# Kernel optimization log

Measured on AMD Instinct MI355X. Metric: run time of the kernel, lower is better.

The kernel has to match this reference:

```python
import jax, jax.numpy as jnp
import numpy as np

N_NODES = 50000
N_EDGES = 1600000
D = 128  # in_dim = hidden = out_dim = 128


def _gat_layer(x, W, b, aW, ab, src, dst, n_nodes):
    # fc: z = x @ W^T + b   (torch Linear convention, W:[out,in])
    z = x @ W.T + b                      # [N, d]
    d = z.shape[1]
    # attn_fc(concat(z_src, z_dst)) decomposed into per-node halves
    a_src = z @ aW[0, :d]                # [N]
    a_dst = z @ aW[0, d:]                # [N]
    e = jax.nn.leaky_relu(a_src[src] + a_dst[dst] + ab[0])  # [E], slope 0.01 (torch default)
    # segment softmax over incoming edges of each dst node
    m = jax.ops.segment_max(e, dst, num_segments=n_nodes)   # [N]
    ex = jnp.exp(e - m[dst])             # [E]
    s = jax.ops.segment_sum(ex, dst, num_segments=n_nodes)  # [N]
    alpha = ex / s[dst]                  # [E]
    # weighted scatter-sum of source features
    h = jax.ops.segment_sum(alpha[:, None] * z[src], dst, num_segments=n_nodes)  # [N, d]
    return h


def setup_inputs() -> dict:
    key = jax.random.key(0)
    ks = jax.random.split(key, 16)
    x = jax.random.normal(ks[0], (N_NODES, D), dtype=jnp.float32)
    src = jax.random.randint(ks[1], (N_EDGES,), 0, N_NODES, dtype=jnp.int32)
    dst = jax.random.randint(ks[2], (N_EDGES,), 0, N_NODES, dtype=jnp.int32)
    inp = {"x": x, "src": src, "dst": dst, "t": 0}
    # 3 GAT layers (128->128, 128->128, 128->128); xavier-ish scale
    for i in range(3):
        base = 3 + 4 * i
        inp[f"W{i}"] = jax.random.normal(ks[base], (D, D), dtype=jnp.float32) * (1.0 / np.sqrt(D))
        inp[f"b{i}"] = jnp.zeros((D,), dtype=jnp.float32)
        inp[f"aW{i}"] = jax.random.normal(ks[base + 1], (1, 2 * D), dtype=jnp.float32) * (1.0 / np.sqrt(2 * D))
        inp[f"ab{i}"] = jnp.zeros((1,), dtype=jnp.float32)
    return inp


def reference(x, src, dst, t, W0, b0, aW0, ab0, W1, b1, aW1, ab1, W2, b2, aW2, ab2):
    n = x.shape[0]
    h = _gat_layer(x, W0, b0, aW0, ab0, src, dst, n)
    h = jax.nn.relu(h)
    h = _gat_layer(h, W1, b1, aW1, ab1, src, dst, n)
    h = jax.nn.relu(h)
    h = _gat_layer(h, W2, b2, aW2, ab2, src, dst, n)
    return h
```

## Files before the change

kernel.cpp:

```cpp
#include <hip/hip_runtime.h>
#include <hip/hip_fp16.h>
#include <math.h>

#define DD 128
#define NBKT 391
#define P1CHUNK 4096
#define P2CAP 8192

typedef _Float16 half8 __attribute__((ext_vector_type(8)));
typedef float floatx4 __attribute__((ext_vector_type(4)));


__global__ __launch_bounds__(256) void fill_zero_i(int* p, int n) {
    int i = blockIdx.x * 256 + threadIdx.x;
    if (i < n) p[i] = 0;
}


__global__ __launch_bounds__(256) void cvt_k(const float* __restrict__ X, __half* __restrict__ Xh, int n8) {
    int i = blockIdx.x * 256 + threadIdx.x;
    if (i >= n8) return;
    const float4* p = reinterpret_cast<const float4*>(X + (size_t)i * 8);
    float4 v0 = p[0], v1 = p[1];
    __half hv[8];
    hv[0] = __float2half(v0.x); hv[1] = __float2half(v0.y);
    hv[2] = __float2half(v0.z); hv[3] = __float2half(v0.w);
    hv[4] = __float2half(v1.x); hv[5] = __float2half(v1.y);
    hv[6] = __float2half(v1.z); hv[7] = __float2half(v1.w);
    *reinterpret_cast<int4*>(Xh + (size_t)i * 8) = *reinterpret_cast<const int4*>(hv);
}

__global__ __launch_bounds__(256) void cvtw3_k(const float* __restrict__ W0, const float* __restrict__ W1,
                                               const float* __restrict__ W2, __half* __restrict__ Wh3) {
    int i = blockIdx.x * 256 + threadIdx.x;
    if (i >= 2048) return;
    const float* Ws[3] = {W0, W1, W2};
#pragma unroll
    for (int m = 0; m < 3; ++m) {
        const float4* p = reinterpret_cast<const float4*>(Ws[m] + (size_t)i * 8);
        float4 v0 = p[0], v1 = p[1];
        __half hv[8];
        hv[0] = __float2half(v0.x); hv[1] = __float2half(v0.y);
        hv[2] = __float2half(v0.z); hv[3] = __float2half(v0.w);
        hv[4] = __float2half(v1.x); hv[5] = __float2half(v1.y);
        hv[6] = __float2half(v1.z); hv[7] = __float2half(v1.w);
        *reinterpret_cast<int4*>(Wh3 + (size_t)m * 16384 + (size_t)i * 8) = *reinterpret_cast<const int4*>(hv);
    }
}


__global__ __launch_bounds__(512) void p1hist_k(const int* __restrict__ dst, int* __restrict__ gcount, int E) {
    __shared__ int lh[NBKT];
    const int tid = threadIdx.x;
    for (int i = tid; i < NBKT; i += 512) lh[i] = 0;
    __syncthreads();
    const int blk0 = blockIdx.x * P1CHUNK;
    const int blkE = min(blk0 + P1CHUNK, E);
    int i0 = blk0 + tid * 8;
    if (i0 + 8 <= blkE) {
        int4 d0 = *reinterpret_cast<const int4*>(dst + i0);
        int4 d1 = *reinterpret_cast<const int4*>(dst + i0 + 4);
        atomicAdd(&lh[d0.x >> 7], 1); atomicAdd(&lh[d0.y >> 7], 1);
        atomicAdd(&lh[d0.z >> 7], 1); atomicAdd(&lh[d0.w >> 7], 1);
        atomicAdd(&lh[d1.x >> 7], 1); atomicAdd(&lh[d1.y >> 7], 1);
        atomicAdd(&lh[d1.z >> 7], 1); atomicAdd(&lh[d1.w >> 7], 1);
    } else {
        for (int j = 0; j < 8; ++j) {
            int i = i0 + j;
            if (i < blkE) atomicAdd(&lh[dst[i] >> 7], 1);
        }
    }
    __syncthreads();
    for (int i = tid; i < NBKT; i += 512)
        if (lh[i]) atomicAdd(&gcount[i], lh[i]);
}


__global__ __launch_bounds__(512) void p1scan_k(const int* __restrict__ gcount, int* __restrict__ bbase,
                                                int* __restrict__ bcur, int E) {
    __shared__ int tmp[512];
    int t = threadIdx.x;
    int v = (t < NBKT) ? gcount[t] : 0;
    tmp[t] = v;
    __syncthreads();
#pragma unroll
    for (int o = 1; o < 512; o <<= 1) {
        int add = (t >= o) ? tmp[t - o] : 0;
        __syncthreads();
        tmp[t] += add;
        __syncthreads();
    }
    if (t <= NBKT) {
        int ex = (t < NBKT) ? (tmp[t] - v) : E;
        bbase[t] = ex;
        if (t < NBKT) bcur[t] = ex;
    }
}


__global__ __launch_bounds__(512) void p1scatter_k(const int* __restrict__ src, const int* __restrict__ dst,
                                                   int* __restrict__ bcur, int2* __restrict__ bufA, int E) {
    __shared__ int lcnt[NBKT];
    __shared__ int lstart[512];
    __shared__ int blkb[NBKT];
    __shared__ int2 stage[P1CHUNK];
    const int tid = threadIdx.x;
    for (int i = tid; i < NBKT; i += 512) lcnt[i] = 0;
    __syncthreads();
    const int blk0 = blockIdx.x * P1CHUNK;
    const int blkE = min(blk0 + P1CHUNK, E);
    const int i0 = blk0 + tid * 8;

    int sv[8], dv[8], bn[8], rk[8], cntT = 0;
    if (i0 + 8 <= blkE) {
        int4 s0 = *reinterpret_cast<const int4*>(src + i0);
        int4 s1 = *reinterpret_cast<const int4*>(src + i0 + 4);
        int4 d0 = *reinterpret_cast<const int4*>(dst + i0);
        int4 d1 = *reinterpret_cast<const int4*>(dst + i0 + 4);
        sv[0] = s0.x; sv[1] = s0.y; sv[2] = s0.z; sv[3] = s0.w;
        sv[4] = s1.x; sv[5] = s1.y; sv[6] = s1.z; sv[7] = s1.w;
        dv[0] = d0.x; dv[1] = d0.y; dv[2] = d0.z; dv[3] = d0.w;
        dv[4] = d1.x; dv[5] = d1.y; dv[6] = d1.z; dv[7] = d1.w;
        cntT = 8;
    } else {
#pragma unroll
        for (int j = 0; j < 8; ++j) {
            int i = i0 + j;
            if (i < blkE) { sv[j] = src[i]; dv[j] = dst[i]; cntT = j + 1; }
        }
    }
#pragma unroll
    for (int j = 0; j < 8; ++j) {
        if (j < cntT) {
            bn[j] = dv[j] >> 7;
            rk[j] = atomicAdd(&lcnt[bn[j]], 1);
        }
    }
    __syncthreads();
    int v = (tid < NBKT) ? lcnt[tid] : 0;
    lstart[tid] = v;
    __syncthreads();
#pragma unroll
    for (int o = 1; o < 512; o <<= 1) {
        int add = (tid >= o) ? lstart[tid - o] : 0;
        __syncthreads();
        lstart[tid] += add;
        __syncthreads();
    }
    lstart[tid] -= v;
    __syncthreads();
    for (int i = tid; i < NBKT; i += 512)
        blkb[i] = lcnt[i] ? atomicAdd(&bcur[i], lcnt[i]) : 0;
#pragma unroll
    for (int j = 0; j < 8; ++j) {
        if (j < cntT) {
            int pos = lstart[bn[j]] + rk[j];
            stage[pos] = make_int2(sv[j], dv[j]);
        }
    }
    __syncthreads();
    const int cnt = blkE - blk0;
    for (int j = tid; j < cnt; j += 512) {
        int2 e = stage[j];
        int b = e.y >> 7;
        bufA[blkb[b] + (j - lstart[b])] = e;
    }
}


__global__ __launch_bounds__(512) void p2sort_k(const int2* __restrict__ bufA, const int* __restrict__ bbase,
                                                int* __restrict__ srcs, int* __restrict__ off, int N, int E) {
    __shared__ int h2[128];
    __shared__ int cur2[128];
    __shared__ int ssrc[P2CAP];
    __shared__ int sdst[P2CAP];
    const int tid = threadIdx.x;
    const int b = blockIdx.x;
    const int base = bbase[b];
    const int cnt = bbase[b + 1] - base;
    for (int i = tid; i < 128; i += 512) h2[i] = 0;
    __syncthreads();
    for (int j = tid; j < cnt; j += 512)
        atomicAdd(&h2[bufA[base + j].y & 127], 1);
    __syncthreads();
    if (tid == 0) {
        int s = 0;
        for (int i = 0; i < 128; ++i) { cur2[i] = s; s += h2[i]; }
    }
    __syncthreads();
    for (int j = tid; j < cnt; j += 512) {
        int2 e = bufA[base + j];
        int p = atomicAdd(&cur2[e.y & 127], 1);
        ssrc[p] = e.x;
        sdst[p] = e.y;
    }
    __syncthreads();
    const int n0 = b * 128;
    const int n1 = min(n0 + 128, N);
    for (int j = tid; j < cnt; j += 512) {
        srcs[base + j] = ssrc[j];
        int d = sdst[j];
        int p = (j == 0) ? (n0 - 1) : sdst[j - 1];
        for (int n = p + 1; n <= d; ++n) off[n] = base + j;
        if (j == cnt - 1)
            for (int n = d + 1; n < n1; ++n) off[n] = base + cnt;
    }
    if (cnt == 0)
        for (int n = n0 + tid; n < n1; n += 512) off[n] = base;
    if (b == NBKT - 1 && tid == 0) off[N] = E;
}


__global__ __launch_bounds__(256) void gemm_k(const __half* __restrict__ Xh, const __half* __restrict__ Wh,
                                              const float* __restrict__ B, const float* __restrict__ aW,
                                              __half* __restrict__ Zh, float* __restrict__ a_src,
                                              float* __restrict__ a_dst, int N) {
    const int tid = threadIdx.x;
    const int wid = tid >> 6;
    const int lane = tid & 63;
    const int cl = lane & 15;
    const int kg = lane >> 4;
    const int row0 = blockIdx.x * 64 + wid * 16;
    int rowA = row0 + cl;
    if (rowA >= N) rowA = N - 1;

    floatx4 acc[8];
#pragma unroll
    for (int t = 0; t < 8; ++t) acc[t] = {0.f, 0.f, 0.f, 0.f};

    const _Float16* Xp = reinterpret_cast<const _Float16*>(Xh);
    const _Float16* Wp = reinterpret_cast<const _Float16*>(Wh);
#pragma unroll
    for (int kk = 0; kk < 4; ++kk) {
        const int kb = kk * 32 + kg * 8;
        half8 av = *reinterpret_cast<const half8*>(Xp + (size_t)rowA * 128 + kb);
#pragma unroll
        for (int t = 0; t < 8; ++t) {
            half8 bv = *reinterpret_cast<const half8*>(Wp + (size_t)(t * 16 + cl) * 128 + kb);
            acc[t] = __builtin_amdgcn_mfma_f32_16x16x32_f16(av, bv, acc[t], 0, 0, 0);
        }
    }
    float pa[4] = {0.f, 0.f, 0.f, 0.f}, pb[4] = {0.f, 0.f, 0.f, 0.f};
#pragma unroll
    for (int t = 0; t < 8; ++t) {
        const int c = t * 16 + cl;
        const float bc = B[c];
        const float w0 = aW[c];
        const float w1 = aW[128 + c];
        const int sl = c >> 5;
        const int cin = c & 31;
#pragma unroll
        for (int j = 0; j < 4; ++j) {
            float z = acc[t][j] + bc;
            pa[j] = fmaf(z, w0, pa[j]);
            pb[j] = fmaf(z, w1, pb[j]);
            int grow = row0 + kg * 4 + j;
            if (grow < N)
                Zh[((size_t)sl * N + grow) * 32 + cin] = __float2half(z);
        }
    }
#pragma unroll
    for (int o = 1; o < 16; o <<= 1) {
#pragma unroll
        for (int j = 0; j < 4; ++j) {
            pa[j] += __shfl_xor(pa[j], o);
            pb[j] += __shfl_xor(pb[j], o);
        }
    }
    if (cl == 0) {
#pragma unroll
        for (int j = 0; j < 4; ++j) {
            int grow = row0 + kg * 4 + j;
            if (grow < N) {
                a_src[grow] = pa[j];
                a_dst[grow] = pb[j];
            }
        }
    }
}


__global__ __launch_bounds__(256) void alpha_k(const float* __restrict__ a_src, const float* __restrict__ a_dst,
                                               const int* __restrict__ off, const int* __restrict__ srcs,
                                               const float* __restrict__ ab, unsigned* __restrict__ pairc, int N) {
    int node = blockIdx.x * 4 + (threadIdx.x >> 6);
    int lane = threadIdx.x & 63;
    if (node >= N) return;
    const int beg = off[node], end = off[node + 1];
    const int deg = end - beg;
    const float adn = a_dst[node] + ab[0];
    if (deg <= 64) {
        int i = beg + lane;
        float p = 0.f; int s = 0;
        if (i < end) {
            s = srcs[i];
            float e = a_src[s] + adn;
            e = (e > 0.f) ? e : 0.01f * e;
            p = __expf(e);
        }
        float psum = p;
#pragma unroll
        for (int o = 1; o < 64; o <<= 1) psum += __shfl_xor(psum, o);
        float inv = (deg > 0) ? 1.0f / psum : 0.0f;
        if (i < end) {
            unsigned ah = __half_as_ushort(__float2half(p * inv));
            pairc[i] = (ah << 16) | (unsigned)s;
        }
    } else {
        float psum = 0.f;
        for (int i = beg + lane; i < end; i += 64) {
            float e = a_src[srcs[i]] + adn;
            e = (e > 0.f) ? e : 0.01f * e;
            psum += __expf(e);
        }
#pragma unroll
        for (int o = 1; o < 64; o <<= 1) psum += __shfl_xor(psum, o);
        const float inv = 1.0f / psum;
        for (int i = beg + lane; i < end; i += 64) {
            int s = srcs[i];
            float e = a_src[s] + adn;
            e = (e > 0.f) ? e : 0.01f * e;
            unsigned ah = __half_as_ushort(__float2half(__expf(e) * inv));
            pairc[i] = (ah << 16) | (unsigned)s;
        }
    }
}


__global__ __launch_bounds__(256) void aggr_k(const __half* __restrict__ Zh, const unsigned* __restrict__ pairc,
                                              const int* __restrict__ off, float* __restrict__ Hf,
                                              __half* __restrict__ Hh, int N) {
    const int slice = blockIdx.x & 3;
    const int lane = threadIdx.x & 63;
    const int wid = threadIdx.x >> 6;
    const int ng = lane >> 4;
    const int node = (blockIdx.x >> 2) * 16 + wid * 4 + ng;
    if (node >= N) return;
    const int eg = (lane >> 2) & 3;
    const int ql = lane & 3;
    const int beg = off[node], end = off[node + 1];
    const __half* Zs = Zh + (size_t)slice * N * 32 + ql * 8;

    float acc[8];
#pragma unroll
    for (int k = 0; k < 8; ++k) acc[k] = 0.f;

    int i = beg + eg;
    for (; i + 4 < end; i += 8) {
        unsigned w0 = pairc[i];
        unsigned w1 = pairc[i + 4];
        int s0 = (int)(w0 & 0xffffu);
        int s1 = (int)(w1 & 0xffffu);
        float a0 = __half2float(__ushort_as_half((unsigned short)(w0 >> 16)));
        float a1 = __half2float(__ushort_as_half((unsigned short)(w1 >> 16)));
        int4 r0 = *reinterpret_cast<const int4*>(Zs + (size_t)s0 * 32);
        int4 r1 = *reinterpret_cast<const int4*>(Zs + (size_t)s1 * 32);
        const __half* h0 = reinterpret_cast<const __half*>(&r0);
        const __half* h1 = reinterpret_cast<const __half*>(&r1);
#pragma unroll
        for (int k = 0; k < 8; ++k) acc[k] = fmaf(a0, __half2float(h0[k]), acc[k]);
#pragma unroll
        for (int k = 0; k < 8; ++k) acc[k] = fmaf(a1, __half2float(h1[k]), acc[k]);
    }
    if (i < end) {
        unsigned w0 = pairc[i];
        int s0 = (int)(w0 & 0xffffu);
        float a0 = __half2float(__ushort_as_half((unsigned short)(w0 >> 16)));
        int4 r0 = *reinterpret_cast<const int4*>(Zs + (size_t)s0 * 32);
        const __half* h0 = reinterpret_cast<const __half*>(&r0);
#pragma unroll
        for (int k = 0; k < 8; ++k) acc[k] = fmaf(a0, __half2float(h0[k]), acc[k]);
    }
#pragma unroll
    for (int o = 4; o <= 8; o <<= 1) {
#pragma unroll
        for (int k = 0; k < 8; ++k) acc[k] += __shfl_xor(acc[k], o);
    }
    if (eg == 0) {
        if (Hh) {
            __half hv[8];
#pragma unroll
            for (int k = 0; k < 8; ++k) hv[k] = __float2half(fmaxf(acc[k], 0.f));
            *reinterpret_cast<int4*>(Hh + (size_t)node * DD + slice * 32 + ql * 8) =
                *reinterpret_cast<const int4*>(hv);
        } else {
            float* out = Hf + (size_t)node * DD + slice * 32 + ql * 8;
#pragma unroll
            for (int k = 0; k < 8; ++k)
                __builtin_nontemporal_store(acc[k], out + k);
        }
    }
}


extern "C" void kernel_launch(void* const* d_in, const int* in_sizes, int n_in,
                              void* d_out, int out_size, void* d_ws, size_t ws_size,
                              hipStream_t stream) {
    const float* x  = (const float*)d_in[0];
    const int* src  = (const int*)d_in[1];
    const int* dst  = (const int*)d_in[2];
    const float* Wl[3]  = {(const float*)d_in[4],  (const float*)d_in[8],  (const float*)d_in[12]};
    const float* bl[3]  = {(const float*)d_in[5],  (const float*)d_in[9],  (const float*)d_in[13]};
    const float* aWl[3] = {(const float*)d_in[6],  (const float*)d_in[10], (const float*)d_in[14]};
    const float* abl[3] = {(const float*)d_in[7],  (const float*)d_in[11], (const float*)d_in[15]};
    const int N = in_sizes[0] / DD;
    const int E = in_sizes[1];

    char* p = (char*)d_ws;
    auto alloc = [&](size_t bytes) -> char* {
        char* r = p;
        p += (bytes + 255) & ~(size_t)255;
        return r;
    };
    __half* Wh3 = (__half*)alloc(3 * 16384 * 2);
    __half* XhA = (__half*)alloc((size_t)N * DD * 2);
    __half* XhB = (__half*)alloc((size_t)N * DD * 2);
    __half* zh  = (__half*)alloc((size_t)N * DD * 2);
    float* asrc = (float*)alloc((size_t)N * 4);
    float* adst = (float*)alloc((size_t)N * 4);
    int* off    = (int*)alloc((size_t)(N + 1) * 4);
    int* srcs   = (int*)alloc((size_t)E * 4);
    unsigned* pairc = (unsigned*)alloc((size_t)E * 4);
    int* gcount = (int*)alloc(512 * 4);
    int* bbase  = (int*)alloc(512 * 4);
    int* bcur   = (int*)alloc(512 * 4);
    int2* bufA  = (int2*)alloc((size_t)E * 8);

    const int NBLK1 = (E + P1CHUNK - 1) / P1CHUNK;

    fill_zero_i<<<2, 256, 0, stream>>>(gcount, 512);
    p1hist_k<<<NBLK1, 512, 0, stream>>>(dst, gcount, E);
    p1scan_k<<<1, 512, 0, stream>>>(gcount, bbase, bcur, E);
    p1scatter_k<<<NBLK1, 512, 0, stream>>>(src, dst, bcur, bufA, E);
    p2sort_k<<<NBKT, 512, 0, stream>>>(bufA, bbase, srcs, off, N, E);
    cvtw3_k<<<8, 256, 0, stream>>>(Wl[0], Wl[1], Wl[2], Wh3);
    const int n8 = N * DD / 8;
    cvt_k<<<(n8 + 255) / 256, 256, 0, stream>>>(x, XhA, n8);

    const int node_blocks = (N + 3) / 4;
    const int aggr_blocks = 4 * ((N + 15) / 16);
    const int gemm_blocks = (N + 63) / 64;

    __half* xin[3]  = {XhA, XhB, XhA};
    __half* hout[3] = {XhB, XhA, nullptr};
    for (int l = 0; l < 3; ++l) {
        gemm_k<<<gemm_blocks, 256, 0, stream>>>(xin[l], Wh3 + (size_t)l * 16384, bl[l], aWl[l],
                                                zh, asrc, adst, N);
        alpha_k<<<node_blocks, 256, 0, stream>>>(asrc, adst, off, srcs, abl[l], pairc, N);
        aggr_k<<<aggr_blocks, 256, 0, stream>>>(zh, pairc, off,
                                                (l == 2) ? (float*)d_out : nullptr, hout[l], N);
    }
}
```

Before: 297.7 us.

## Pack edge src/dst into 32-bit words, vectorize GEMM epilogue, fuse conversion kernels

New measurement: 299.4 us. About the same (+0.6%).

```diff
diff --git a/kernel.cpp b/kernel.cpp
--- a/kernel.cpp
+++ b/kernel.cpp
@@ -17,34 +17,33 @@
 }
 
 
-__global__ __launch_bounds__(256) void cvt_k(const float* __restrict__ X, __half* __restrict__ Xh, int n8) {
+__global__ __launch_bounds__(256) void cvt_all_k(const float* __restrict__ X, __half* __restrict__ Xh, int n8,
+                                                 const float* __restrict__ W0, const float* __restrict__ W1,
+                                                 const float* __restrict__ W2, __half* __restrict__ Wh3) {
     int i = blockIdx.x * 256 + threadIdx.x;
-    if (i >= n8) return;
-    const float4* p = reinterpret_cast<const float4*>(X + (size_t)i * 8);
-    float4 v0 = p[0], v1 = p[1];
-    __half hv[8];
-    hv[0] = __float2half(v0.x); hv[1] = __float2half(v0.y);
-    hv[2] = __float2half(v0.z); hv[3] = __float2half(v0.w);
-    hv[4] = __float2half(v1.x); hv[5] = __float2half(v1.y);
-    hv[6] = __float2half(v1.z); hv[7] = __float2half(v1.w);
-    *reinterpret_cast<int4*>(Xh + (size_t)i * 8) = *reinterpret_cast<const int4*>(hv);
-}
-
-__global__ __launch_bounds__(256) void cvtw3_k(const float* __restrict__ W0, const float* __restrict__ W1,
-                                               const float* __restrict__ W2, __half* __restrict__ Wh3) {
-    int i = blockIdx.x * 256 + threadIdx.x;
-    if (i >= 2048) return;
-    const float* Ws[3] = {W0, W1, W2};
-#pragma unroll
-    for (int m = 0; m < 3; ++m) {
-        const float4* p = reinterpret_cast<const float4*>(Ws[m] + (size_t)i * 8);
+    if (i < n8) {
+        const float4* p = reinterpret_cast<const float4*>(X + (size_t)i * 8);
         float4 v0 = p[0], v1 = p[1];
         __half hv[8];
         hv[0] = __float2half(v0.x); hv[1] = __float2half(v0.y);
         hv[2] = __float2half(v0.z); hv[3] = __float2half(v0.w);
         hv[4] = __float2half(v1.x); hv[5] = __float2half(v1.y);
         hv[6] = __float2half(v1.z); hv[7] = __float2half(v1.w);
-        *reinterpret_cast<int4*>(Wh3 + (size_t)m * 16384 + (size_t)i * 8) = *reinterpret_cast<const int4*>(hv);
+        *reinterpret_cast<int4*>(Xh + (size_t)i * 8) = *reinterpret_cast<const int4*>(hv);
+    }
+    if (i < 2048) {
+        const float* Ws[3] = {W0, W1, W2};
+#pragma unroll
+        for (int m = 0; m < 3; ++m) {
+            const float4* p = reinterpret_cast<const float4*>(Ws[m] + (size_t)i * 8);
+            float4 v0 = p[0], v1 = p[1];
+            __half hv[8];
+            hv[0] = __float2half(v0.x); hv[1] = __float2half(v0.y);
+            hv[2] = __float2half(v0.z); hv[3] = __float2half(v0.w);
+            hv[4] = __float2half(v1.x); hv[5] = __float2half(v1.y);
+            hv[6] = __float2half(v1.z); hv[7] = __float2half(v1.w);
+            *reinterpret_cast<int4*>(Wh3 + (size_t)m * 16384 + (size_t)i * 8) = *reinterpret_cast<const int4*>(hv);
+        }
     }
 }
 
@@ -99,11 +98,11 @@
 
 
 __global__ __launch_bounds__(512) void p1scatter_k(const int* __restrict__ src, const int* __restrict__ dst,
-                                                   int* __restrict__ bcur, int2* __restrict__ bufA, int E) {
+                                                   int* __restrict__ bcur, unsigned* __restrict__ bufA, int E) {
     __shared__ int lcnt[NBKT];
     __shared__ int lstart[512];
     __shared__ int blkb[NBKT];
-    __shared__ int2 stage[P1CHUNK];
+    __shared__ unsigned stage[P1CHUNK];
     const int tid = threadIdx.x;
     for (int i = tid; i < NBKT; i += 512) lcnt[i] = 0;
     __syncthreads();
@@ -155,25 +154,25 @@
     for (int j = 0; j < 8; ++j) {
         if (j < cntT) {
             int pos = lstart[bn[j]] + rk[j];
-            stage[pos] = make_int2(sv[j], dv[j]);
+            stage[pos] = ((unsigned)dv[j] << 16) | (unsigned)sv[j];
         }
     }
     __syncthreads();
     const int cnt = blkE - blk0;
     for (int j = tid; j < cnt; j += 512) {
-        int2 e = stage[j];
-        int b = e.y >> 7;
-        bufA[blkb[b] + (j - lstart[b])] = e;
-    }
-}
-
-
-__global__ __launch_bounds__(512) void p2sort_k(const int2* __restrict__ bufA, const int* __restrict__ bbase,
+        unsigned w = stage[j];
+        int b = (int)(w >> 23);
+        bufA[blkb[b] + (j - lstart[b])] = w;
+    }
+}
+
+
+__global__ __launch_bounds__(512) void p2sort_k(const unsigned* __restrict__ bufA, const int* __restrict__ bbase,
                                                 int* __restrict__ srcs, int* __restrict__ off, int N, int E) {
     __shared__ int h2[128];
     __shared__ int cur2[128];
     __shared__ int ssrc[P2CAP];
-    __shared__ int sdst[P2CAP];
+    __shared__ short sdst[P2CAP];
     const int tid = threadIdx.x;
     const int b = blockIdx.x;
     const int base = bbase[b];
@@ -181,7 +180,7 @@
     for (int i = tid; i < 128; i += 512) h2[i] = 0;
     __syncthreads();
     for (int j = tid; j < cnt; j += 512)
-        atomicAdd(&h2[bufA[base + j].y & 127], 1);
+        atomicAdd(&h2[(bufA[base + j] >> 16) & 127], 1);
     __syncthreads();
     if (tid == 0) {
         int s = 0;
@@ -189,24 +188,26 @@
     }
     __syncthreads();
     for (int j = tid; j < cnt; j += 512) {
-        int2 e = bufA[base + j];
-        int p = atomicAdd(&cur2[e.y & 127], 1);
-        ssrc[p] = e.x;
-        sdst[p] = e.y;
+        unsigned w = bufA[base + j];
+        int ld = (int)((w >> 16) & 127);
+        int p = atomicAdd(&cur2[ld], 1);
+        ssrc[p] = (int)(w & 0xffffu);
+        sdst[p] = (short)ld;
     }
     __syncthreads();
     const int n0 = b * 128;
     const int n1 = min(n0 + 128, N);
+    const int nloc = n1 - n0;
     for (int j = tid; j < cnt; j += 512) {
         srcs[base + j] = ssrc[j];
         int d = sdst[j];
-        int p = (j == 0) ? (n0 - 1) : sdst[j - 1];
-        for (int n = p + 1; n <= d; ++n) off[n] = base + j;
+        int pd = (j == 0) ? -1 : (int)sdst[j - 1];
+        for (int n = pd + 1; n <= d; ++n) off[n0 + n] = base + j;
         if (j == cnt - 1)
-            for (int n = d + 1; n < n1; ++n) off[n] = base + cnt;
+            for (int n = d + 1; n < nloc; ++n) off[n0 + n] = base + cnt;
     }
     if (cnt == 0)
-        for (int n = n0 + tid; n < n1; n += 512) off[n] = base;
+        for (int n = tid; n < nloc; n += 512) off[n0 + n] = base;
     if (b == NBKT - 1 && tid == 0) off[N] = E;
 }
 
@@ -237,45 +238,35 @@
 #pragma unroll
         for (int t = 0; t < 8; ++t) {
             half8 bv = *reinterpret_cast<const half8*>(Wp + (size_t)(t * 16 + cl) * 128 + kb);
-            acc[t] = __builtin_amdgcn_mfma_f32_16x16x32_f16(av, bv, acc[t], 0, 0, 0);
-        }
-    }
-    float pa[4] = {0.f, 0.f, 0.f, 0.f}, pb[4] = {0.f, 0.f, 0.f, 0.f};
+            acc[t] = __builtin_amdgcn_mfma_f32_16x16x32_f16(bv, av, acc[t], 0, 0, 0);
+        }
+    }
+    const int grow = row0 + cl;
+    float pa = 0.f, pb = 0.f;
 #pragma unroll
     for (int t = 0; t < 8; ++t) {
-        const int c = t * 16 + cl;
-        const float bc = B[c];
-        const float w0 = aW[c];
-        const float w1 = aW[128 + c];
-        const int sl = c >> 5;
-        const int cin = c & 31;
+        const int cb = t * 16 + 4 * kg;
+        __half hv[4];
 #pragma unroll
         for (int j = 0; j < 4; ++j) {
-            float z = acc[t][j] + bc;
-            pa[j] = fmaf(z, w0, pa[j]);
-            pb[j] = fmaf(z, w1, pb[j]);
-            int grow = row0 + kg * 4 + j;
-            if (grow < N)
-                Zh[((size_t)sl * N + grow) * 32 + cin] = __float2half(z);
-        }
-    }
-#pragma unroll
-    for (int o = 1; o < 16; o <<= 1) {
-#pragma unroll
-        for (int j = 0; j < 4; ++j) {
-            pa[j] += __shfl_xor(pa[j], o);
-            pb[j] += __shfl_xor(pb[j], o);
-        }
-    }
-    if (cl == 0) {
-#pragma unroll
-        for (int j = 0; j < 4; ++j) {
-            int grow = row0 + kg * 4 + j;
-            if (grow < N) {
-                a_src[grow] = pa[j];
-                a_dst[grow] = pb[j];
-            }
-        }
+            const int c = cb + j;
+            float z = acc[t][j] + B[c];
+            pa = fmaf(z, aW[c], pa);
+            pb = fmaf(z, aW[128 + c], pb);
+            hv[j] = __float2half(z);
+        }
+        if (grow < N) {
+            const int sl = t >> 1;
+            const int cin = 16 * (t & 1) + 4 * kg;
+            *reinterpret_cast<int2*>(Zh + ((size_t)sl * N + grow) * 32 + cin) =
+                *reinterpret_cast<const int2*>(hv);
+        }
+    }
+    pa += __shfl_xor(pa, 16); pb += __shfl_xor(pb, 16);
+    pa += __shfl_xor(pa, 32); pb += __shfl_xor(pb, 32);
+    if (kg == 0 && grow < N) {
+        a_src[grow] = pa;
+        a_dst[grow] = pb;
     }
 }
 
@@ -424,7 +415,7 @@
     int* gcount = (int*)alloc(512 * 4);
     int* bbase  = (int*)alloc(512 * 4);
     int* bcur   = (int*)alloc(512 * 4);
-    int2* bufA  = (int2*)alloc((size_t)E * 8);
+    unsigned* bufA = (unsigned*)alloc((size_t)E * 4);
 
     const int NBLK1 = (E + P1CHUNK - 1) / P1CHUNK;
 
@@ -433,9 +424,8 @@
     p1scan_k<<<1, 512, 0, stream>>>(gcount, bbase, bcur, E);
     p1scatter_k<<<NBLK1, 512, 0, stream>>>(src, dst, bcur, bufA, E);
     p2sort_k<<<NBKT, 512, 0, stream>>>(bufA, bbase, srcs, off, N, E);
-    cvtw3_k<<<8, 256, 0, stream>>>(Wl[0], Wl[1], Wl[2], Wh3);
     const int n8 = N * DD / 8;
-    cvt_k<<<(n8 + 255) / 256, 256, 0, stream>>>(x, XhA, n8);
+    cvt_all_k<<<(n8 + 255) / 256, 256, 0, stream>>>(x, XhA, n8, Wl[0], Wl[1], Wl[2], Wh3);
 
     const int node_blocks = (N + 3) / 4;
     const int aggr_blocks = 4 * ((N + 15) / 16);
```
